# Kernel optimization log

Hardware: AMD Instinct MI355X
Metric: run time of the kernel (lower is better)

The kernel has to match this reference:

```python
import jax, jax.numpy as jnp
import numpy as np

STRIDE = 1
PAD = 1

def setup_inputs() -> dict:
    key = jax.random.key(0)
    k1, k2 = jax.random.split(key)
    x = jax.random.normal(k1, (32, 128, 56, 56), dtype=jnp.float32)
    weight = jax.random.normal(k2, (256, 128, 3, 3), dtype=jnp.float32) * 0.1
    b = jnp.zeros((256,), dtype=jnp.float32)
    return {"x": x, "weight": weight, "b": b}

def reference(x, weight, b):
    # Binarize weights with sign (matches torch.sign: sign(0)=0), then plain conv2d.
    bw = jnp.sign(weight)
    out = jax.lax.conv_general_dilated(
        x, bw,
        window_strides=(STRIDE, STRIDE),
        padding=((PAD, PAD), (PAD, PAD)),
        dimension_numbers=("NCHW", "OIHW", "NCHW"),
    )
    return out + b[None, :, None, None]
```

## Files before the change

### kernel.cpp

```cpp
#include <hip/hip_runtime.h>
#include <hip/hip_bf16.h>

typedef __attribute__((ext_vector_type(8))) short bf16x8;
typedef __attribute__((ext_vector_type(4))) float f32x4;

#define CIN   128
#define COUT  256
#define NIMG  32
#define HWDIM 56
#define HPAD  58
#define KTOT  1152
#define HWIMG 3136
#define MTOT  100352
#define BK    64
#define NT    18
#define NS    36

__device__ __forceinline__ void gload16(const void* g, void* l) {
  __builtin_amdgcn_global_load_lds((const __attribute__((address_space(1))) void*)g,
                                   (__attribute__((address_space(3))) void*)l,
                                   16, 0, 0);
}

__global__ __launch_bounds__(256)
void prep_all(const float* __restrict__ x, const float* __restrict__ w,
              __hip_bfloat16* __restrict__ xp, __hip_bfloat16* __restrict__ wtf) {
  __shared__ float tile[CIN * 57];
  const int bid = blockIdx.x;
  const int t = threadIdx.x;
  if (bid < NIMG * HPAD) {
    const int n = bid / HPAD;
    const int h = bid - n * HPAD;
    __hip_bfloat16* dstrow = xp + ((size_t)n * HPAD + h) * HPAD * CIN;
    int4 z; z.x = 0; z.y = 0; z.z = 0; z.w = 0;
    if (h == 0 || h == HPAD - 1) {
      for (int i = t; i < (HPAD * CIN) / 8; i += 256)
        reinterpret_cast<int4*>(dstrow)[i] = z;
      return;
    }
    const float* src = x + (size_t)n * CIN * HWIMG + (size_t)(h - 1) * HWDIM;
    for (int i = t; i < CIN * HWDIM; i += 256) {
      int c = i / HWDIM;
      int wd = i - c * HWDIM;
      tile[c * 57 + wd] = src[(size_t)c * HWIMG + wd];
    }
    if (t < 32) {
      int side = t >> 4;
      reinterpret_cast<int4*>(dstrow + (side ? (HPAD - 1) : 0) * CIN)[t & 15] = z;
    }
    __syncthreads();
    __hip_bfloat16* dst = dstrow + CIN;
    for (int o = t; o < HWDIM * 64; o += 256) {
      int wd = o >> 6;
      int c = (o & 63) * 2;
      __hip_bfloat162 pr;
      pr.x = __float2bfloat16(tile[c * 57 + wd]);
      pr.y = __float2bfloat16(tile[(c + 1) * 57 + wd]);
      *reinterpret_cast<__hip_bfloat162*>(dst + (size_t)wd * CIN + c) = pr;
    }
  } else {
    int o = (bid - NIMG * HPAD) * 256 + t;
    int cout = o / KTOT;
    int k = o - cout * KTOT;
    int tap = k >> 7;
    int cin = k & 127;
    float v = w[((size_t)cout * CIN + cin) * 9 + tap];
    int dst = (((cout >> 4) * NS + (k >> 5)) * 64 + (cout & 15) + (((k >> 3) & 3) << 4)) * 8 + (k & 7);
    wtf[dst] = __float2bfloat16(v > 0.f ? 1.f : (v < 0.f ? -1.f : 0.f));
  }
}

__global__ __launch_bounds__(256, 3)
void bconv(const short* __restrict__ xp, const short* __restrict__ wtf,
           const float* __restrict__ bias, float* __restrict__ out) {
  __shared__ short lx[2][128 * BK];

  const int tid  = threadIdx.x;
  const int lane = tid & 63;
  const int wv   = tid >> 6;
  const int wm   = wv >> 1;
  const int wn   = wv & 1;

  const int myid = blockIdx.y * 784 + blockIdx.x;
  const int sid  = (myid & 7) * 196 + (myid >> 3);
  const int s0   = (sid >> 1) * 128;
  const int f0   = (sid & 1) * 128;

  const int srow = tid >> 3;
  const int slot = tid & 7;
  const int swz  = slot ^ (srow & 7);

  int xoff[4];
#pragma unroll
  for (int r = 0; r < 4; ++r) {
    int m  = s0 + r * 32 + srow;
    int n  = m / HWIMG;
    int hw = m - n * HWIMG;
    int h  = hw / HWDIM;
    int w  = hw - h * HWDIM;
    xoff[r] = ((n * HPAD + h) * HPAD + w) * CIN + swz * 8;
  }

  const short* wbase = wtf + (size_t)((f0 >> 4) + wm * 4) * NS * 512 + lane * 8;

  f32x4 acc[4][4] = {};
  bf16x8 af[4][2], bx[4][2];

#define AF_LOAD(T) \
  _Pragma("unroll") for (int f = 0; f < 4; ++f) \
  _Pragma("unroll") for (int ksub = 0; ksub < 2; ++ksub) \
    af[f][ksub] = *(const bf16x8*)(wbase + ((size_t)f * NS + (T) * 2 + ksub) * 512);

#define XKO(T) ((((T) >> 1) / 3 * HPAD + ((T) >> 1) % 3) * CIN + ((T) & 1) * BK)

#define STAGE_B(C, T) \
  _Pragma("unroll") for (int r = 0; r < 4; ++r) \
    gload16(xp + xoff[r] + XKO(T), &lx[C][(r * 32 + wv * 8) * BK]);

  STAGE_B(0, 0)
  AF_LOAD(0)

  const int rlo = lane & 15;
  const int kq  = lane >> 4;
  const int swr = rlo & 7;

  for (int t = 0; t < NT; ++t) {
    const int cur = t & 1;
    asm volatile("s_waitcnt vmcnt(8)" ::: "memory");
    __builtin_amdgcn_s_barrier();

    if (t + 1 < NT) { STAGE_B(cur ^ 1, t + 1) }

#pragma unroll
    for (int f = 0; f < 4; ++f)
#pragma unroll
      for (int ksub = 0; ksub < 2; ++ksub)
        bx[f][ksub] = *(const bf16x8*)&lx[cur][(wn * 64 + f * 16 + rlo) * BK + ((ksub * 4 + kq) ^ swr) * 8];

#pragma unroll
    for (int kk = 0; kk < 2; ++kk)
#pragma unroll
      for (int fm = 0; fm < 4; ++fm)
#pragma unroll
        for (int fn = 0; fn < 4; ++fn)
          acc[fm][fn] = __builtin_amdgcn_mfma_f32_16x16x32_bf16(
              bx[fn][kk], af[fm][kk], acc[fm][fn], 0, 0, 0);

    if (t + 1 < NT) { AF_LOAD(t + 1) }
  }

  const int col = lane & 15;
  const int rg  = lane >> 4;
  int nb[4], hwb[4];
#pragma unroll
  for (int fn = 0; fn < 4; ++fn) {
    int m16 = s0 + wn * 64 + fn * 16;
    int n = m16 / HWIMG;
    nb[fn]  = n;
    hwb[fn] = m16 - n * HWIMG + rg * 4;
  }
#pragma unroll
  for (int fm = 0; fm < 4; ++fm) {
    int cc = f0 + wm * 64 + fm * 16 + col;
    float bv = bias[cc];
#pragma unroll
    for (int fn = 0; fn < 4; ++fn) {
      float4 v;
      v.x = acc[fm][fn][0] + bv;
      v.y = acc[fm][fn][1] + bv;
      v.z = acc[fm][fn][2] + bv;
      v.w = acc[fm][fn][3] + bv;
      *reinterpret_cast<float4*>(out + ((size_t)nb[fn] * COUT + cc) * HWIMG + hwb[fn]) = v;
    }
  }
#undef AF_LOAD
#undef XKO
#undef STAGE_B
}

extern "C" void kernel_launch(void* const* d_in, const int* in_sizes, int n_in,
                              void* d_out, int out_size, void* d_ws, size_t ws_size,
                              hipStream_t stream) {
  const float* x = (const float*)d_in[0];
  const float* w = (const float*)d_in[1];
  const float* b = (const float*)d_in[2];
  float* out = (float*)d_out;

  const size_t xp_elems = (size_t)NIMG * HPAD * HPAD * CIN;
  __hip_bfloat16* xp  = (__hip_bfloat16*)d_ws;
  __hip_bfloat16* wtf = xp + xp_elems;

  prep_all<<<NIMG * HPAD + (COUT * KTOT) / 256, 256, 0, stream>>>(x, w, xp, wtf);

  dim3 grid(MTOT / 128, COUT / 128);
  bconv<<<grid, 256, 0, stream>>>((const short*)xp, (const short*)wtf, b, out);
}
```

Baseline: 93.53 us.

## Double-buffer weight fragments and split LDS reads across MFMA k-halves

Unrolls the K loop by two with ping-pong weight register buffers, so next-step weight fragments are loaded before the current MFMAs rather than after them. The LDS reads for the second k-half are moved between the two MFMA groups to overlap with compute. A sched_barrier pins this ordering. The barrier moves to the end of each step with a full vmcnt(0) wait, which may serialize the global prefetch more than the previous partial wait. The extra weight buffer also raises register pressure.

```diff
diff --git a/kernel.cpp b/kernel.cpp
--- a/kernel.cpp
+++ b/kernel.cpp
@@ -104,49 +104,49 @@
   const short* wbase = wtf + (size_t)((f0 >> 4) + wm * 4) * NS * 512 + lane * 8;
 
   f32x4 acc[4][4] = {};
-  bf16x8 af[4][2], bx[4][2];
-
-#define AF_LOAD(T) \
-  _Pragma("unroll") for (int f = 0; f < 4; ++f) \
-  _Pragma("unroll") for (int ksub = 0; ksub < 2; ++ksub) \
-    af[f][ksub] = *(const bf16x8*)(wbase + ((size_t)f * NS + (T) * 2 + ksub) * 512);
+  bf16x8 afP[4][2], afQ[4][2];
 
 #define XKO(T) ((((T) >> 1) / 3 * HPAD + ((T) >> 1) % 3) * CIN + ((T) & 1) * BK)
-
 #define STAGE_B(C, T) \
   _Pragma("unroll") for (int r = 0; r < 4; ++r) \
     gload16(xp + xoff[r] + XKO(T), &lx[C][(r * 32 + wv * 8) * BK]);
-
-  STAGE_B(0, 0)
-  AF_LOAD(0)
+#define AF_LOAD(DST, T) \
+  _Pragma("unroll") for (int f = 0; f < 4; ++f) \
+  _Pragma("unroll") for (int ks = 0; ks < 2; ++ks) \
+    DST[f][ks] = *(const bf16x8*)(wbase + ((size_t)f * NS + (T) * 2 + ks) * 512);
 
   const int rlo = lane & 15;
   const int kq  = lane >> 4;
   const int swr = rlo & 7;
 
-  for (int t = 0; t < NT; ++t) {
-    const int cur = t & 1;
-    asm volatile("s_waitcnt vmcnt(8)" ::: "memory");
-    __builtin_amdgcn_s_barrier();
+#define STEP(T, AFU, AFN) { \
+    const int cur = (T) & 1; \
+    if ((T) + 1 < NT) { STAGE_B(cur ^ 1, (T) + 1) } \
+    bf16x8 bx0[4], bx1[4]; \
+    _Pragma("unroll") for (int f = 0; f < 4; ++f) \
+      bx0[f] = *(const bf16x8*)&lx[cur][(wn * 64 + f * 16 + rlo) * BK + (kq ^ swr) * 8]; \
+    if ((T) + 1 < NT) { AF_LOAD(AFN, (T) + 1) } \
+    __builtin_amdgcn_sched_barrier(0); \
+    _Pragma("unroll") for (int fm = 0; fm < 4; ++fm) \
+    _Pragma("unroll") for (int fn = 0; fn < 4; ++fn) \
+      acc[fm][fn] = __builtin_amdgcn_mfma_f32_16x16x32_bf16(bx0[fn], AFU[fm][0], acc[fm][fn], 0, 0, 0); \
+    _Pragma("unroll") for (int f = 0; f < 4; ++f) \
+      bx1[f] = *(const bf16x8*)&lx[cur][(wn * 64 + f * 16 + rlo) * BK + ((4 + kq) ^ swr) * 8]; \
+    _Pragma("unroll") for (int fm = 0; fm < 4; ++fm) \
+    _Pragma("unroll") for (int fn = 0; fn < 4; ++fn) \
+      acc[fm][fn] = __builtin_amdgcn_mfma_f32_16x16x32_bf16(bx1[fn], AFU[fm][1], acc[fm][fn], 0, 0, 0); \
+    asm volatile("s_waitcnt vmcnt(0)" ::: "memory"); \
+    __builtin_amdgcn_s_barrier(); \
+  }
 
-    if (t + 1 < NT) { STAGE_B(cur ^ 1, t + 1) }
+  AF_LOAD(afP, 0)
+  STAGE_B(0, 0)
+  asm volatile("s_waitcnt vmcnt(0)" ::: "memory");
+  __builtin_amdgcn_s_barrier();
 
-#pragma unroll
-    for (int f = 0; f < 4; ++f)
-#pragma unroll
-      for (int ksub = 0; ksub < 2; ++ksub)
-        bx[f][ksub] = *(const bf16x8*)&lx[cur][(wn * 64 + f * 16 + rlo) * BK + ((ksub * 4 + kq) ^ swr) * 8];
-
-#pragma unroll
-    for (int kk = 0; kk < 2; ++kk)
-#pragma unroll
-      for (int fm = 0; fm < 4; ++fm)
-#pragma unroll
-        for (int fn = 0; fn < 4; ++fn)
-          acc[fm][fn] = __builtin_amdgcn_mfma_f32_16x16x32_bf16(
-              bx[fn][kk], af[fm][kk], acc[fm][fn], 0, 0, 0);
-
-    if (t + 1 < NT) { AF_LOAD(t + 1) }
+  for (int t = 0; t < NT; t += 2) {
+    STEP(t,     afP, afQ)
+    STEP(t + 1, afQ, afP)
   }
 
   const int col = lane & 15;
@@ -173,9 +173,10 @@
       *reinterpret_cast<float4*>(out + ((size_t)nb[fn] * COUT + cc) * HWIMG + hwb[fn]) = v;
     }
   }
-#undef AF_LOAD
 #undef XKO
 #undef STAGE_B
+#undef AF_LOAD
+#undef STEP
 }
 
 extern "C" void kernel_launch(void* const* d_in, const int* in_sizes, int n_in,
```

New measurement: 174.8 us. 86.9% more time.
